# Kernel optimization log

Measured on AMD Instinct MI355X. Metric: run time of the kernel, lower is better.

Reference implementation:

```python
import jax, jax.numpy as jnp
import numpy as np

HEADS = 8
DIM_HEAD = 64
WINDOW = 128
PERSIST = 4
EPS = 1.1920929e-07  # torch nn.RMSNorm default eps = finfo(fp32).eps


def _rope_freqs(n, d, dtype):
    inv_freq = 1.0 / (10000.0 ** (jnp.arange(0, d, 2, dtype=jnp.float32) / d))
    freqs = jnp.arange(n, dtype=jnp.float32)[:, None] * inv_freq[None, :]  # [n, d/2]
    freqs = jnp.repeat(freqs, 2, axis=-1)  # interleaved repeat -> [n, d]
    return jnp.cos(freqs).astype(dtype), jnp.sin(freqs).astype(dtype)


def _rotate_half(x):
    # interleaved pairs (x0,x1),(x2,x3)... -> (-x1,x0),(-x3,x2)...
    x = x.reshape(*x.shape[:-1], -1, 2)
    x1, x2 = x[..., 0], x[..., 1]
    return jnp.stack((-x2, x1), axis=-1).reshape(*x.shape[:-2], -1)


def setup_inputs() -> dict:
    key = jax.random.key(0)
    k1, k2, k3 = jax.random.split(key, 3)
    B, N, D = 1, 4096, 1024
    dim_inner = HEADS * DIM_HEAD  # 512
    return {
        "seq": jax.random.normal(k1, (B, N, D), dtype=jnp.float32),
        "g": jnp.ones((D,), dtype=jnp.float32),
        "w_qkv": jax.random.normal(k2, (D, 3 * dim_inner), dtype=jnp.float32) * 0.02,
        "w_out": jax.random.normal(k3, (dim_inner, D), dtype=jnp.float32) * 0.02,
    }


def reference(seq, g, w_qkv, w_out):
    B, N, D = seq.shape
    H, Dh = HEADS, DIM_HEAD

    # RMSNorm
    x = seq * jax.lax.rsqrt(jnp.mean(seq * seq, axis=-1, keepdims=True) + EPS) * g

    # QKV projection -> [B, H, N, Dh]
    qkv = x @ w_qkv
    q, k, v = jnp.split(qkv, 3, axis=-1)
    to_heads = lambda t: t.reshape(B, N, H, Dh).transpose(0, 2, 1, 3)
    q, k, v = map(to_heads, (q, k, v))

    # rotary embeddings (same positions for q and k)
    cos, sin = _rope_freqs(N, Dh, q.dtype)
    q = q * cos + _rotate_half(q) * sin
    k = k * cos + _rotate_half(k) * sin

    # causal & (persist | sliding-window) mask
    idx = jnp.arange(N)
    dist = idx[:, None] - idx[None, :]
    mask = (dist >= 0) & ((idx[None, :] < PERSIST) | (dist <= WINDOW))  # [N, N]

    scale = Dh ** -0.5
    scores = jnp.einsum("bhid,bhjd->bhij", q, k) * scale
    neg = -jnp.finfo(scores.dtype).max
    scores = jnp.where(mask[None, None], scores, neg)
    attn = jax.nn.softmax(scores, axis=-1)
    out = jnp.einsum("bhij,bhjd->bhid", attn, v)

    out = out.transpose(0, 2, 1, 3).reshape(B, N, H * Dh)
    return out @ w_out
```

## Files before the change

kernel.cpp:

```cpp
#include <hip/hip_runtime.h>
#include <hip/hip_bf16.h>
#include <math.h>

#define SEQ    4096
#define DMODEL 1024
#define NHEADS 8
#define DH     64
#define DINNER 512
#define NQKV   1536
#define WINDOW 128
#define PERSIST 4
#define EPS 1.1920929e-07f

typedef unsigned short u16;
typedef unsigned int   u32;
typedef __bf16  bf16_8 __attribute__((ext_vector_type(8)));
typedef float   f32x4  __attribute__((ext_vector_type(4)));

union BV { bf16_8 v; u16 s[8]; };

__device__ __forceinline__ float b2f(u16 u) {
    union { u32 i; float f; } v; v.i = ((u32)u) << 16; return v.f;
}
__device__ __forceinline__ u16 f2b(float f) {
    union { float f; u32 i; } v; v.f = f;
    u32 i = v.i;
    u32 r = (i + 0x7fffu + ((i >> 16) & 1u)) >> 16;
    return (u16)r;
}

#define GLD16(gp, lp) __builtin_amdgcn_global_load_lds( \
    (const __attribute__((address_space(1))) void*)(gp), \
    (__attribute__((address_space(3))) void*)(lp), 16, 0, 0)

__device__ __forceinline__ void transpose_tile(const float* __restrict__ src,
                                               u16* __restrict__ dst,
                                               int K, int N, int bn, int bk,
                                               u16 (*t)[65], int tid) {
    int r = tid >> 4, c4 = (tid & 15) * 4;
    #pragma unroll
    for (int it = 0; it < 4; it++) {
        int row = r + it * 16;
        float4 v = *(const float4*)(src + (size_t)(bk + row) * N + bn + c4);
        t[row][c4 + 0] = f2b(v.x);
        t[row][c4 + 1] = f2b(v.y);
        t[row][c4 + 2] = f2b(v.z);
        t[row][c4 + 3] = f2b(v.w);
    }
    __syncthreads();
    #pragma unroll
    for (int it = 0; it < 4; it++) {
        int n = r + it * 16;
        u16* d = dst + (size_t)(bn + n) * K + bk + c4;
        uint2 o;
        o.x = (u32)t[c4 + 0][n] | ((u32)t[c4 + 1][n] << 16);
        o.y = (u32)t[c4 + 2][n] | ((u32)t[c4 + 3][n] << 16);
        *(uint2*)d = o;
    }
}

__global__ __launch_bounds__(256) void prep_kernel(const float* __restrict__ wqkv,
                                                   const float* __restrict__ wout,
                                                   const float* __restrict__ seq,
                                                   const float* __restrict__ g,
                                                   u16* __restrict__ wqkv_bt,
                                                   u16* __restrict__ wout_bt,
                                                   u16* __restrict__ x) {
    __shared__ u16 t[64][65];
    __shared__ float wsum[4];
    int b = blockIdx.x, tid = threadIdx.x;
    if (b < 384) {
        transpose_tile(wqkv, wqkv_bt, DMODEL, NQKV, (b % 24) * 64, (b / 24) * 64, t, tid);
    } else if (b < 512) {
        int bb = b - 384;
        transpose_tile(wout, wout_bt, DINNER, DMODEL, (bb % 16) * 64, (bb / 16) * 64, t, tid);
    } else {
        int row = b - 512;
        float4 v = *(const float4*)(seq + (size_t)row * DMODEL + tid * 4);
        float ss = v.x*v.x + v.y*v.y + v.z*v.z + v.w*v.w;
        #pragma unroll
        for (int o = 32; o > 0; o >>= 1) ss += __shfl_xor(ss, o);
        if ((tid & 63) == 0) wsum[tid >> 6] = ss;
        __syncthreads();
        float tot = wsum[0] + wsum[1] + wsum[2] + wsum[3];
        float rstd = rsqrtf(tot * (1.0f / DMODEL) + EPS);
        float4 gv = *(const float4*)(g + tid * 4);
        uint2 o;
        o.x = (u32)f2b(v.x * rstd * gv.x) | ((u32)f2b(v.y * rstd * gv.y) << 16);
        o.y = (u32)f2b(v.z * rstd * gv.z) | ((u32)f2b(v.w * rstd * gv.w) << 16);
        *(uint2*)(x + (size_t)row * DMODEL + tid * 4) = o;
    }
}

template <int MODE, int NTW, int KTOT>
__global__ __launch_bounds__(256, 2) void gemm2_kernel(const u16* __restrict__ A,
                                                       const u16* __restrict__ Bt,
                                                       u16* __restrict__ C0,
                                                       u16* __restrict__ C1,
                                                       u16* __restrict__ C2,
                                                       float* __restrict__ Cf,
                                                       int M, int N, int K) {
    constexpr int BN  = NTW * 32;
    constexpr int GPW = BN / 32;
    __shared__ u16 As[2][128 * 64];
    __shared__ u16 Bs[2][BN * 64];
    int bx = blockIdx.x, by = blockIdx.y, tid = threadIdx.x;
    int lane = tid & 63, wave = tid >> 6;
    int m16 = lane & 15, quad = lane >> 4;
    int rw0 = (wave & 1) * 64, cw0 = (wave >> 1) * (NTW * 16);

    f32x4 acc[4][NTW];
    #pragma unroll
    for (int mt = 0; mt < 4; mt++)
        #pragma unroll
        for (int nt = 0; nt < NTW; nt++) acc[mt][nt] = (f32x4){0.f, 0.f, 0.f, 0.f};

    int lrow = lane & 7, lkc = lane >> 3;
    const u16* Ag = A  + (size_t)(by * 128 + lrow) * KTOT + lkc * 8;
    const u16* Bg = Bt + (size_t)(bx * BN  + lrow) * KTOT + lkc * 8;

    for (int k0 = 0; k0 < KTOT; k0 += 128) {
        #pragma unroll
        for (int hb = 0; hb < 2; hb++) {
            #pragma unroll
            for (int r = 0; r < 4; r++) {
                int gg = wave * 4 + r;
                GLD16(Ag + (size_t)(gg * 8) * KTOT + k0 + hb * 64, As[hb] + gg * 512);
            }
            #pragma unroll
            for (int r = 0; r < GPW; r++) {
                int gg = wave * GPW + r;
                GLD16(Bg + (size_t)(gg * 8) * KTOT + k0 + hb * 64, Bs[hb] + gg * 512);
            }
        }
        __syncthreads();

        #pragma unroll
        for (int hb = 0; hb < 2; hb++) {
            #pragma unroll
            for (int kk = 0; kk < 2; kk++) {
                int kc = kk * 4 + quad;
                bf16_8 afr[4], bfr[NTW];
                #pragma unroll
                for (int mt = 0; mt < 4; mt++) {
                    int row = rw0 + mt * 16 + m16;
                    afr[mt] = *(const bf16_8*)(As[hb] + (row >> 3) * 512 + kc * 64 + (row & 7) * 8);
                }
                #pragma unroll
                for (int nt = 0; nt < NTW; nt++) {
                    int col = cw0 + nt * 16 + m16;
                    bfr[nt] = *(const bf16_8*)(Bs[hb] + (col >> 3) * 512 + kc * 64 + (col & 7) * 8);
                }
                #pragma unroll
                for (int mt = 0; mt < 4; mt++)
                    #pragma unroll
                    for (int nt = 0; nt < NTW; nt++)
                        acc[mt][nt] = __builtin_amdgcn_mfma_f32_16x16x32_bf16(afr[mt], bfr[nt], acc[mt][nt], 0, 0, 0);
            }
        }
        __syncthreads();
    }

    #pragma unroll
    for (int nt = 0; nt < NTW; nt++) {
        int col = bx * BN + cw0 + nt * 16 + m16;
        if (MODE == 0) {
            int tens = col >> 9, hh = (col >> 6) & 7, dh = col & 63;
            if (tens == 2) {
                #pragma unroll
                for (int mt = 0; mt < 4; mt++) {
                    int nb = by * 128 + rw0 + mt * 16 + quad * 4;
                    uint2 o;
                    o.x = (u32)f2b(acc[mt][nt][0]) | ((u32)f2b(acc[mt][nt][1]) << 16);
                    o.y = (u32)f2b(acc[mt][nt][2]) | ((u32)f2b(acc[mt][nt][3]) << 16);
                    *(uint2*)(C2 + ((size_t)(hh * DH + dh)) * SEQ + nb) = o;
                }
            } else {
                int tt = (col & 63) >> 1;
                float inv = exp2f(-(float)(2 * tt) * (13.287712379549449f / 64.0f));
                bool odd = (col & 1);
                u16* dst = (tens == 0) ? C0 : C1;
                #pragma unroll
                for (int mt = 0; mt < 4; mt++) {
                    #pragma unroll
                    for (int r = 0; r < 4; r++) {
                        int row = by * 128 + rw0 + mt * 16 + quad * 4 + r;
                        float own = acc[mt][nt][r];
                        float part = __shfl_xor(own, 1);
                        float s, c;
                        __sincosf((float)row * inv, &s, &c);
                        float val = odd ? (own * c + part * s) : (own * c - part * s);
                        dst[((size_t)hh * SEQ + row) * DH + dh] = f2b(val);
                    }
                }
            }
        } else {
            #pragma unroll
            for (int mt = 0; mt < 4; mt++) {
                #pragma unroll
                for (int r = 0; r < 4; r++) {
                    int row = by * 128 + rw0 + mt * 16 + quad * 4 + r;
                    Cf[(size_t)row * N + col] = acc[mt][nt][r];
                }
            }
        }
    }
}

#define AROWS 208
#define KLD   72
#define PLD   168
#define VLD   222

__global__ __launch_bounds__(256, 2) void attn_mfma(const u16* __restrict__ Q,
                                                    const u16* __restrict__ Kt,
                                                    const u16* __restrict__ Vg,
                                                    u16* __restrict__ O) {
    __shared__ __align__(16) char smem[29952 + 64 * VLD * 2];
    u16* Ks = (u16*)smem;
    u16* Ps = (u16*)smem;
    u16* Vt = (u16*)(smem + 29952);
    int i0 = blockIdx.x * 64, h = blockIdx.y;
    int tid = threadIdx.x, wave = tid >> 6, lane = tid & 63;
    int m16 = lane & 15, quad = lane >> 4;
    int smin = (i0 > WINDOW) ? i0 - WINDOW : 0;

    for (int idx = tid; idx < AROWS * 8; idx += 256) {
        int row = idx >> 3, c = idx & 7;
        int j = (row < 16) ? row : (smin + row - 16);
        *(bf16_8*)(Ks + row * KLD + c * 8) =
            *(const bf16_8*)(Kt + ((size_t)h * SEQ + j) * DH + c * 8);
    }
    for (int idx = tid; idx < 64 * 26; idx += 256) {
        int d = idx / 26, c = idx - d * 26;
        int t0 = c * 8;
        int n0 = (c < 2) ? t0 : (smin + t0 - 16);
        *(bf16_8*)(Vt + d * VLD + t0) =
            *(const bf16_8*)(Vg + ((size_t)(h * DH + d)) * SEQ + n0);
    }

    int iw0 = i0 + wave * 16;
    int iq = iw0 + m16;
    const u16* qrow = Q + ((size_t)h * SEQ + iq) * DH;
    bf16_8 qa = *(const bf16_8*)(qrow + quad * 8);
    bf16_8 qb = *(const bf16_8*)(qrow + 32 + quad * 8);
    __syncthreads();

    int start_w = (iw0 > WINDOW) ? iw0 - WINDOW : 0;
    int Dw = start_w - smin;
    int tlast = 31 + iw0 - start_w;
    int nch = (tlast >> 4) + 1;
    int nk32 = (tlast >> 5) + 1;

    f32x4 S[10];
    __builtin_amdgcn_s_setprio(1);
    #pragma unroll
    for (int c = 0; c < 10; c++) {
        if (c < nch) {
            int t = c * 16 + m16;
            int row = (c == 0) ? t : (t + Dw);
            const u16* kp = Ks + row * KLD;
            bf16_8 kb0 = *(const bf16_8*)(kp + quad * 8);
            bf16_8 kb1 = *(const bf16_8*)(kp + 32 + quad * 8);
            f32x4 s = (f32x4){0.f, 0.f, 0.f, 0.f};
            s = __builtin_amdgcn_mfma_f32_16x16x32_bf16(qa, kb0, s, 0, 0, 0);
            s = __builtin_amdgcn_mfma_f32_16x16x32_bf16(qb, kb1, s, 0, 0, 0);
            S[c] = s;
        }
    }
    __builtin_amdgcn_s_setprio(0);
    __syncthreads();

    float mrow[4] = {-1e30f, -1e30f, -1e30f, -1e30f};
    #pragma unroll
    for (int c = 0; c < 10; c++) {
        if (c < nch) {
            int t = c * 16 + m16;
            int j = (c == 0) ? t : (start_w + t - 16);
            #pragma unroll
            for (int r = 0; r < 4; r++) {
                int i = iw0 + quad * 4 + r;
                bool valid = (c == 0) ? (j < PERSIST && j < start_w)
                                      : (j <= i && (i - j <= WINDOW || j < PERSIST));
                float sv = valid ? S[c][r] * 0.125f : -1e30f;
                S[c][r] = sv;
                mrow[r] = fmaxf(mrow[r], sv);
            }
        }
    }
    #pragma unroll
    for (int r = 0; r < 4; r++) {
        #pragma unroll
        for (int o = 1; o < 16; o <<= 1) mrow[r] = fmaxf(mrow[r], __shfl_xor(mrow[r], o));
    }
    float srow[4] = {0.f, 0.f, 0.f, 0.f};
    #pragma unroll
    for (int c = 0; c < 10; c++) {
        if (c < nch) {
            #pragma unroll
            for (int r = 0; r < 4; r++) {
                float p = __expf(S[c][r] - mrow[r]);
                S[c][r] = p;
                srow[r] += p;
            }
        }
    }
    #pragma unroll
    for (int r = 0; r < 4; r++) {
        #pragma unroll
        for (int o = 1; o < 16; o <<= 1) srow[r] += __shfl_xor(srow[r], o);
    }

    u16* pw = Ps + wave * 16 * PLD;
    #pragma unroll
    for (int c = 0; c < 10; c++) {
        #pragma unroll
        for (int r = 0; r < 4; r++) {
            u16 val = (c < nch) ? f2b(S[c][r]) : (u16)0;
            pw[(quad * 4 + r) * PLD + c * 16 + m16] = val;
        }
    }

    f32x4 oacc[4];
    #pragma unroll
    for (int nt = 0; nt < 4; nt++) oacc[nt] = (f32x4){0.f, 0.f, 0.f, 0.f};
    __builtin_amdgcn_s_setprio(1);
    #pragma unroll
    for (int c2 = 0; c2 < 5; c2++) {
        if (c2 < nk32) {
            bf16_8 af = *(const bf16_8*)(pw + m16 * PLD + c2 * 32 + quad * 8);
            int kbase = c2 * 32 + quad * 8;
            int rowb = (kbase < 16) ? kbase : (kbase + Dw);
            #pragma unroll
            for (int nt = 0; nt < 4; nt++) {
                int d = nt * 16 + m16;
                bf16_8 bv = *(const bf16_8*)(Vt + d * VLD + rowb);
                oacc[nt] = __builtin_amdgcn_mfma_f32_16x16x32_bf16(af, bv, oacc[nt], 0, 0, 0);
            }
        }
    }
    __builtin_amdgcn_s_setprio(0);

    float rinv[4];
    #pragma unroll
    for (int r = 0; r < 4; r++) rinv[r] = 1.0f / srow[r];
    #pragma unroll
    for (int nt = 0; nt < 4; nt++) {
        #pragma unroll
        for (int r = 0; r < 4; r++) {
            int i = iw0 + quad * 4 + r;
            O[(size_t)i * DINNER + h * DH + nt * 16 + m16] = f2b(oacc[nt][r] * rinv[r]);
        }
    }
}

extern "C" void kernel_launch(void* const* d_in, const int* in_sizes, int n_in,
                              void* d_out, int out_size, void* d_ws, size_t ws_size,
                              hipStream_t stream) {
    const float* seq  = (const float*)d_in[0];
    const float* g    = (const float*)d_in[1];
    const float* wqkv = (const float*)d_in[2];
    const float* wout = (const float*)d_in[3];
    float* out = (float*)d_out;

    char* ws = (char*)d_ws;
    u16* x       = (u16*)(ws);
    u16* q       = (u16*)(ws + 8ll  * 1024 * 1024);
    u16* k       = (u16*)(ws + 12ll * 1024 * 1024);
    u16* v       = (u16*)(ws + 16ll * 1024 * 1024);
    u16* att     = (u16*)(ws + 20ll * 1024 * 1024);
    u16* wqkv_bt = (u16*)(ws + 24ll * 1024 * 1024);
    u16* wout_bt = (u16*)(ws + 27ll * 1024 * 1024);

    prep_kernel<<<4608, 256, 0, stream>>>(wqkv, wout, seq, g, wqkv_bt, wout_bt, x);

    dim3 g1(NQKV / 96, SEQ / 128);
    gemm2_kernel<0, 3, DMODEL><<<g1, 256, 0, stream>>>(x, wqkv_bt, q, k, v, nullptr, SEQ, NQKV, DMODEL);

    dim3 g2(SEQ / 64, NHEADS);
    attn_mfma<<<g2, 256, 0, stream>>>(q, k, v, att);

    dim3 g3(DMODEL / 64, SEQ / 128);
    gemm2_kernel<1, 2, DINNER><<<g3, 256, 0, stream>>>(att, wout_bt, nullptr, nullptr, nullptr, out, SEQ, DMODEL, DINNER);
}
```

Measured before the change: 140.6 us.

## Fuse all four stages into one persistent kernel with grid barriers

```diff
diff --git a/kernel.cpp b/kernel.cpp
--- a/kernel.cpp
+++ b/kernel.cpp
@@ -11,17 +11,13 @@
 #define WINDOW 128
 #define PERSIST 4
 #define EPS 1.1920929e-07f
+#define NBLK 512
 
 typedef unsigned short u16;
 typedef unsigned int   u32;
 typedef __bf16  bf16_8 __attribute__((ext_vector_type(8)));
 typedef float   f32x4  __attribute__((ext_vector_type(4)));
 
-union BV { bf16_8 v; u16 s[8]; };
-
-__device__ __forceinline__ float b2f(u16 u) {
-    union { u32 i; float f; } v; v.i = ((u32)u) << 16; return v.f;
-}
 __device__ __forceinline__ u16 f2b(float f) {
     union { float f; u32 i; } v; v.f = f;
     u32 i = v.i;
@@ -32,6 +28,22 @@
 #define GLD16(gp, lp) __builtin_amdgcn_global_load_lds( \
     (const __attribute__((address_space(1))) void*)(gp), \
     (__attribute__((address_space(3))) void*)(lp), 16, 0, 0)
+
+__device__ __forceinline__ void grid_barrier(u32* cnt, u32* flag, int tid) {
+    __syncthreads();
+    if (tid == 0) {
+        u32 old = __hip_atomic_fetch_add(cnt, 1u, __ATOMIC_ACQ_REL, __HIP_MEMORY_SCOPE_AGENT);
+        if (old == NBLK - 1u) {
+            __hip_atomic_store(flag, 1u, __ATOMIC_RELEASE, __HIP_MEMORY_SCOPE_AGENT);
+        } else {
+            while (__hip_atomic_load(flag, __ATOMIC_RELAXED, __HIP_MEMORY_SCOPE_AGENT) == 0u) {
+                __builtin_amdgcn_s_sleep(2);
+            }
+            (void)__hip_atomic_load(flag, __ATOMIC_ACQUIRE, __HIP_MEMORY_SCOPE_AGENT);
+        }
+    }
+    __syncthreads();
+}
 
 __device__ __forceinline__ void transpose_tile(const float* __restrict__ src,
                                                u16* __restrict__ dst,
@@ -59,52 +71,18 @@
     }
 }
 
-__global__ __launch_bounds__(256) void prep_kernel(const float* __restrict__ wqkv,
-                                                   const float* __restrict__ wout,
-                                                   const float* __restrict__ seq,
-                                                   const float* __restrict__ g,
-                                                   u16* __restrict__ wqkv_bt,
-                                                   u16* __restrict__ wout_bt,
-                                                   u16* __restrict__ x) {
-    __shared__ u16 t[64][65];
-    __shared__ float wsum[4];
-    int b = blockIdx.x, tid = threadIdx.x;
-    if (b < 384) {
-        transpose_tile(wqkv, wqkv_bt, DMODEL, NQKV, (b % 24) * 64, (b / 24) * 64, t, tid);
-    } else if (b < 512) {
-        int bb = b - 384;
-        transpose_tile(wout, wout_bt, DINNER, DMODEL, (bb % 16) * 64, (bb / 16) * 64, t, tid);
-    } else {
-        int row = b - 512;
-        float4 v = *(const float4*)(seq + (size_t)row * DMODEL + tid * 4);
-        float ss = v.x*v.x + v.y*v.y + v.z*v.z + v.w*v.w;
-        #pragma unroll
-        for (int o = 32; o > 0; o >>= 1) ss += __shfl_xor(ss, o);
-        if ((tid & 63) == 0) wsum[tid >> 6] = ss;
-        __syncthreads();
-        float tot = wsum[0] + wsum[1] + wsum[2] + wsum[3];
-        float rstd = rsqrtf(tot * (1.0f / DMODEL) + EPS);
-        float4 gv = *(const float4*)(g + tid * 4);
-        uint2 o;
-        o.x = (u32)f2b(v.x * rstd * gv.x) | ((u32)f2b(v.y * rstd * gv.y) << 16);
-        o.y = (u32)f2b(v.z * rstd * gv.z) | ((u32)f2b(v.w * rstd * gv.w) << 16);
-        *(uint2*)(x + (size_t)row * DMODEL + tid * 4) = o;
-    }
-}
-
-template <int MODE, int NTW, int KTOT>
-__global__ __launch_bounds__(256, 2) void gemm2_kernel(const u16* __restrict__ A,
-                                                       const u16* __restrict__ Bt,
-                                                       u16* __restrict__ C0,
-                                                       u16* __restrict__ C1,
-                                                       u16* __restrict__ C2,
-                                                       float* __restrict__ Cf,
-                                                       int M, int N, int K) {
+template <int MODE, int NTW, int KTOT, int NOUT>
+__device__ __forceinline__ void gemm_body(const u16* __restrict__ A,
+                                          const u16* __restrict__ Bt,
+                                          u16* __restrict__ C0,
+                                          u16* __restrict__ C1,
+                                          u16* __restrict__ C2,
+                                          float* __restrict__ Cf,
+                                          int bx, int by, int tid, char* smem) {
     constexpr int BN  = NTW * 32;
     constexpr int GPW = BN / 32;
-    __shared__ u16 As[2][128 * 64];
-    __shared__ u16 Bs[2][BN * 64];
-    int bx = blockIdx.x, by = blockIdx.y, tid = threadIdx.x;
+    u16* As = (u16*)smem;
+    u16* Bs = (u16*)(smem + 2 * 128 * 64 * 2);
     int lane = tid & 63, wave = tid >> 6;
     int m16 = lane & 15, quad = lane >> 4;
     int rw0 = (wave & 1) * 64, cw0 = (wave >> 1) * (NTW * 16);
@@ -125,12 +103,12 @@
             #pragma unroll
             for (int r = 0; r < 4; r++) {
                 int gg = wave * 4 + r;
-                GLD16(Ag + (size_t)(gg * 8) * KTOT + k0 + hb * 64, As[hb] + gg * 512);
+                GLD16(Ag + (size_t)(gg * 8) * KTOT + k0 + hb * 64, As + hb * 8192 + gg * 512);
             }
             #pragma unroll
             for (int r = 0; r < GPW; r++) {
                 int gg = wave * GPW + r;
-                GLD16(Bg + (size_t)(gg * 8) * KTOT + k0 + hb * 64, Bs[hb] + gg * 512);
+                GLD16(Bg + (size_t)(gg * 8) * KTOT + k0 + hb * 64, Bs + hb * (BN * 64) + gg * 512);
             }
         }
         __syncthreads();
@@ -144,12 +122,12 @@
                 #pragma unroll
                 for (int mt = 0; mt < 4; mt++) {
                     int row = rw0 + mt * 16 + m16;
-                    afr[mt] = *(const bf16_8*)(As[hb] + (row >> 3) * 512 + kc * 64 + (row & 7) * 8);
+                    afr[mt] = *(const bf16_8*)(As + hb * 8192 + (row >> 3) * 512 + kc * 64 + (row & 7) * 8);
                 }
                 #pragma unroll
                 for (int nt = 0; nt < NTW; nt++) {
                     int col = cw0 + nt * 16 + m16;
-                    bfr[nt] = *(const bf16_8*)(Bs[hb] + (col >> 3) * 512 + kc * 64 + (col & 7) * 8);
+                    bfr[nt] = *(const bf16_8*)(Bs + hb * (BN * 64) + (col >> 3) * 512 + kc * 64 + (col & 7) * 8);
                 }
                 #pragma unroll
                 for (int mt = 0; mt < 4; mt++)
@@ -200,7 +178,7 @@
                 #pragma unroll
                 for (int r = 0; r < 4; r++) {
                     int row = by * 128 + rw0 + mt * 16 + quad * 4 + r;
-                    Cf[(size_t)row * N + col] = acc[mt][nt][r];
+                    Cf[(size_t)row * NOUT + col] = acc[mt][nt][r];
                 }
             }
         }
@@ -212,16 +190,15 @@
 #define PLD   168
 #define VLD   222
 
-__global__ __launch_bounds__(256, 2) void attn_mfma(const u16* __restrict__ Q,
-                                                    const u16* __restrict__ Kt,
-                                                    const u16* __restrict__ Vg,
-                                                    u16* __restrict__ O) {
-    __shared__ __align__(16) char smem[29952 + 64 * VLD * 2];
+__device__ __forceinline__ void attn_body(const u16* __restrict__ Q,
+                                          const u16* __restrict__ Kt,
+                                          const u16* __restrict__ Vg,
+                                          u16* __restrict__ O,
+                                          int i0, int h, int tid, char* smem) {
     u16* Ks = (u16*)smem;
     u16* Ps = (u16*)smem;
     u16* Vt = (u16*)(smem + 29952);
-    int i0 = blockIdx.x * 64, h = blockIdx.y;
-    int tid = threadIdx.x, wave = tid >> 6, lane = tid & 63;
+    int wave = tid >> 6, lane = tid & 63;
     int m16 = lane & 15, quad = lane >> 4;
     int smin = (i0 > WINDOW) ? i0 - WINDOW : 0;
 
@@ -354,6 +331,60 @@
     }
 }
 
+__global__ __launch_bounds__(256, 2) void fused_kernel(const float* __restrict__ seq,
+                                                       const float* __restrict__ g,
+                                                       const float* __restrict__ wqkv,
+                                                       const float* __restrict__ wout,
+                                                       u16* __restrict__ x,
+                                                       u16* __restrict__ q,
+                                                       u16* __restrict__ k,
+                                                       u16* __restrict__ v,
+                                                       u16* __restrict__ att,
+                                                       u16* __restrict__ wqkv_bt,
+                                                       u16* __restrict__ wout_bt,
+                                                       u32* __restrict__ bars,
+                                                       float* __restrict__ out) {
+    __shared__ __align__(16) char smem[58368];
+    int bid = blockIdx.x, tid = threadIdx.x;
+
+    {
+        u16 (*t)[65] = (u16(*)[65])smem;
+        float* wsum = (float*)(smem + 8320);
+        if (bid < 384) {
+            transpose_tile(wqkv, wqkv_bt, DMODEL, NQKV, (bid % 24) * 64, (bid / 24) * 64, t, tid);
+        } else {
+            int bb = bid - 384;
+            transpose_tile(wout, wout_bt, DINNER, DMODEL, (bb % 16) * 64, (bb / 16) * 64, t, tid);
+        }
+        for (int rr = 0; rr < 8; rr++) {
+            int row = bid * 8 + rr;
+            float4 vv = *(const float4*)(seq + (size_t)row * DMODEL + tid * 4);
+            float ss = vv.x*vv.x + vv.y*vv.y + vv.z*vv.z + vv.w*vv.w;
+            #pragma unroll
+            for (int o = 32; o > 0; o >>= 1) ss += __shfl_xor(ss, o);
+            if ((tid & 63) == 0) wsum[tid >> 6] = ss;
+            __syncthreads();
+            float tot = wsum[0] + wsum[1] + wsum[2] + wsum[3];
+            float rstd = rsqrtf(tot * (1.0f / DMODEL) + EPS);
+            float4 gv = *(const float4*)(g + tid * 4);
+            uint2 o;
+            o.x = (u32)f2b(vv.x * rstd * gv.x) | ((u32)f2b(vv.y * rstd * gv.y) << 16);
+            o.y = (u32)f2b(vv.z * rstd * gv.z) | ((u32)f2b(vv.w * rstd * gv.w) << 16);
+            *(uint2*)(x + (size_t)row * DMODEL + tid * 4) = o;
+            __syncthreads();
+        }
+    }
+    grid_barrier(bars + 0, bars + 32, tid);
+
+    gemm_body<0, 3, DMODEL, NQKV>(x, wqkv_bt, q, k, v, nullptr, bid & 15, bid >> 4, tid, smem);
+    grid_barrier(bars + 64, bars + 96, tid);
+
+    attn_body(q, k, v, att, (bid & 63) * 64, bid >> 6, tid, smem);
+    grid_barrier(bars + 128, bars + 160, tid);
+
+    gemm_body<1, 2, DINNER, DMODEL>(att, wout_bt, nullptr, nullptr, nullptr, out, bid & 15, bid >> 4, tid, smem);
+}
+
 extern "C" void kernel_launch(void* const* d_in, const int* in_sizes, int n_in,
                               void* d_out, int out_size, void* d_ws, size_t ws_size,
                               hipStream_t stream) {
@@ -371,15 +402,12 @@
     u16* att     = (u16*)(ws + 20ll * 1024 * 1024);
     u16* wqkv_bt = (u16*)(ws + 24ll * 1024 * 1024);
     u16* wout_bt = (u16*)(ws + 27ll * 1024 * 1024);
-
-    prep_kernel<<<4608, 256, 0, stream>>>(wqkv, wout, seq, g, wqkv_bt, wout_bt, x);
-
-    dim3 g1(NQKV / 96, SEQ / 128);
-    gemm2_kernel<0, 3, DMODEL><<<g1, 256, 0, stream>>>(x, wqkv_bt, q, k, v, nullptr, SEQ, NQKV, DMODEL);
-
-    dim3 g2(SEQ / 64, NHEADS);
-    attn_mfma<<<g2, 256, 0, stream>>>(q, k, v, att);
-
-    dim3 g3(DMODEL / 64, SEQ / 128);
-    gemm2_kernel<1, 2, DINNER><<<g3, 256, 0, stream>>>(att, wout_bt, nullptr, nullptr, nullptr, out, SEQ, DMODEL, DINNER);
-}
+    u32* bars    = (u32*)(ws + 28ll * 1024 * 1024);
+
+    hipMemsetAsync((void*)bars, 0, 1024, stream);
+
+    void* kargs[] = {(void*)&seq, (void*)&g, (void*)&wqkv, (void*)&wout,
+                     (void*)&x, (void*)&q, (void*)&k, (void*)&v, (void*)&att,
+                     (void*)&wqkv_bt, (void*)&wout_bt, (void*)&bars, (void*)&out};
+    hipLaunchKernel((void*)fused_kernel, dim3(NBLK), dim3(256), kargs, 0, stream);
+}
```

After: 200.1 us. 42.3% more time.

## Double-buffer GEMM K-tiles to overlap global-to-LDS loads with MFMA compute

Applied to the files above, without the earlier changes.

```diff
diff --git a/kernel.cpp b/kernel.cpp
--- a/kernel.cpp
+++ b/kernel.cpp
@@ -17,11 +17,6 @@
 typedef __bf16  bf16_8 __attribute__((ext_vector_type(8)));
 typedef float   f32x4  __attribute__((ext_vector_type(4)));
 
-union BV { bf16_8 v; u16 s[8]; };
-
-__device__ __forceinline__ float b2f(u16 u) {
-    union { u32 i; float f; } v; v.i = ((u32)u) << 16; return v.f;
-}
 __device__ __forceinline__ u16 f2b(float f) {
     union { float f; u32 i; } v; v.f = f;
     u32 i = v.i;
@@ -102,6 +97,7 @@
                                                        int M, int N, int K) {
     constexpr int BN  = NTW * 32;
     constexpr int GPW = BN / 32;
+    constexpr int NT  = KTOT / 64;
     __shared__ u16 As[2][128 * 64];
     __shared__ u16 Bs[2][BN * 64];
     int bx = blockIdx.x, by = blockIdx.y, tid = threadIdx.x;
@@ -119,47 +115,62 @@
     const u16* Ag = A  + (size_t)(by * 128 + lrow) * KTOT + lkc * 8;
     const u16* Bg = Bt + (size_t)(bx * BN  + lrow) * KTOT + lkc * 8;
 
-    for (int k0 = 0; k0 < KTOT; k0 += 128) {
-        #pragma unroll
-        for (int hb = 0; hb < 2; hb++) {
-            #pragma unroll
-            for (int r = 0; r < 4; r++) {
-                int gg = wave * 4 + r;
-                GLD16(Ag + (size_t)(gg * 8) * KTOT + k0 + hb * 64, As[hb] + gg * 512);
-            }
-            #pragma unroll
-            for (int r = 0; r < GPW; r++) {
-                int gg = wave * GPW + r;
-                GLD16(Bg + (size_t)(gg * 8) * KTOT + k0 + hb * 64, Bs[hb] + gg * 512);
-            }
-        }
-        __syncthreads();
-
-        #pragma unroll
-        for (int hb = 0; hb < 2; hb++) {
-            #pragma unroll
-            for (int kk = 0; kk < 2; kk++) {
-                int kc = kk * 4 + quad;
-                bf16_8 afr[4], bfr[NTW];
+    auto stage_tile = [&](int tt, int bb) {
+        int k0 = tt * 64;
+        u16* Ad = (u16*)As + bb * 8192;
+        u16* Bd = (u16*)Bs + bb * (BN * 64);
+        #pragma unroll
+        for (int r = 0; r < 4; r++) {
+            int gg = wave * 4 + r;
+            GLD16(Ag + (size_t)(gg * 8) * KTOT + k0, Ad + gg * 512);
+        }
+        #pragma unroll
+        for (int r = 0; r < GPW; r++) {
+            int gg = wave * GPW + r;
+            GLD16(Bg + (size_t)(gg * 8) * KTOT + k0, Bd + gg * 512);
+        }
+    };
+    auto compute_tile = [&](int bb) {
+        const u16* Ab = (const u16*)As + bb * 8192;
+        const u16* Bb = (const u16*)Bs + bb * (BN * 64);
+        #pragma unroll
+        for (int kk = 0; kk < 2; kk++) {
+            int kc = kk * 4 + quad;
+            bf16_8 afr[4], bfr[NTW];
+            #pragma unroll
+            for (int mt = 0; mt < 4; mt++) {
+                int row = rw0 + mt * 16 + m16;
+                afr[mt] = *(const bf16_8*)(Ab + (row >> 3) * 512 + kc * 64 + (row & 7) * 8);
+            }
+            #pragma unroll
+            for (int nt = 0; nt < NTW; nt++) {
+                int col = cw0 + nt * 16 + m16;
+                bfr[nt] = *(const bf16_8*)(Bb + (col >> 3) * 512 + kc * 64 + (col & 7) * 8);
+            }
+            #pragma unroll
+            for (int mt = 0; mt < 4; mt++)
                 #pragma unroll
-                for (int mt = 0; mt < 4; mt++) {
-                    int row = rw0 + mt * 16 + m16;
-                    afr[mt] = *(const bf16_8*)(As[hb] + (row >> 3) * 512 + kc * 64 + (row & 7) * 8);
-                }
-                #pragma unroll
-                for (int nt = 0; nt < NTW; nt++) {
-                    int col = cw0 + nt * 16 + m16;
-                    bfr[nt] = *(const bf16_8*)(Bs[hb] + (col >> 3) * 512 + kc * 64 + (col & 7) * 8);
-                }
-                #pragma unroll
-                for (int mt = 0; mt < 4; mt++)
-                    #pragma unroll
-                    for (int nt = 0; nt < NTW; nt++)
-                        acc[mt][nt] = __builtin_amdgcn_mfma_f32_16x16x32_bf16(afr[mt], bfr[nt], acc[mt][nt], 0, 0, 0);
-            }
-        }
-        __syncthreads();
-    }
+                for (int nt = 0; nt < NTW; nt++)
+                    acc[mt][nt] = __builtin_amdgcn_mfma_f32_16x16x32_bf16(afr[mt], bfr[nt], acc[mt][nt], 0, 0, 0);
+        }
+    };
+
+    stage_tile(0, 0);
+    #pragma unroll 1
+    for (int t = 0; t < NT - 1; t++) {
+        int cur = t & 1;
+        stage_tile(t + 1, cur ^ 1);
+        if constexpr (NTW == 3) asm volatile("s_waitcnt vmcnt(7)" ::: "memory");
+        else                    asm volatile("s_waitcnt vmcnt(6)" ::: "memory");
+        __builtin_amdgcn_s_barrier();
+        __builtin_amdgcn_sched_barrier(0);
+        compute_tile(cur);
+        __builtin_amdgcn_s_barrier();
+    }
+    asm volatile("s_waitcnt vmcnt(0)" ::: "memory");
+    __builtin_amdgcn_s_barrier();
+    __builtin_amdgcn_sched_barrier(0);
+    compute_tile((NT - 1) & 1);
 
     #pragma unroll
     for (int nt = 0; nt < NTW; nt++) {
```

Measured after the change: 139.9 us. About the same (-0.5%).
